# Performance work log

Measured on AMD Instinct MI355X. Metric: run time of the kernel, lower is better.

## Reference

```python
import jax, jax.numpy as jnp
import numpy as np

B, N, DIN, DOUT, H = 4, 2048, 512, 512, 8
HD = DOUT // H


def setup_inputs() -> dict:
    key = jax.random.key(0)
    ks = jax.random.split(key, 8)
    x = jax.random.normal(ks[0], (B, N, DIN), dtype=jnp.float32)
    mask = jax.random.randint(ks[1], (B, 1, N, N), 0, 2, dtype=jnp.int32)
    s = 1.0 / np.sqrt(DIN)
    Wq = jax.random.uniform(ks[2], (DOUT, DIN), jnp.float32, -s, s)
    Wk = jax.random.uniform(ks[3], (DOUT, DIN), jnp.float32, -s, s)
    Wv = jax.random.uniform(ks[4], (DOUT, DIN), jnp.float32, -s, s)
    bq = jax.random.uniform(ks[5], (DOUT,), jnp.float32, -s, s)
    bk = jax.random.uniform(ks[6], (DOUT,), jnp.float32, -s, s)
    bv = jax.random.uniform(ks[7], (DOUT,), jnp.float32, -s, s)
    return {"x": x, "Wq": Wq, "bq": bq, "Wk": Wk, "bk": bk, "Wv": Wv, "bv": bv, "mask": mask}


def reference(x, Wq, bq, Wk, bk, Wv, bv, mask):
    b, n, _ = x.shape
    # torch Linear: y = x @ W.T + b ; split heads -> [b, h, n, hd]
    def proj(W, bias):
        y = jnp.einsum('bnd,od->bno', x, W) + bias
        return y.reshape(b, n, H, HD).transpose(0, 2, 1, 3)
    Q, K, V = proj(Wq, bq), proj(Wk, bk), proj(Wv, bv)
    scores = jnp.einsum('bhnd,bhmd->bhnm', Q, K) / np.sqrt(HD).astype(np.float32)
    scores = jnp.where(mask == 0, jnp.float32(-1e9), scores)
    attn = jax.nn.softmax(scores, axis=-1)
    ctx = jnp.einsum('bhnm,bhmd->bhnd', attn, V)
    ctx = ctx.transpose(0, 2, 1, 3).reshape(b, n, DOUT)
    return jax.nn.elu(ctx)
```

## Files before the change

kernel.cpp:

```cpp
#include <hip/hip_runtime.h>
#include <math.h>
#include <stdint.h>

#define CB 4
#define CN 2048
#define CDIN 512
#define CDOUT 512
#define CH 8
#define CHD 64
#define CM (CB * CN)
#define CBH (CB * CH)
#define NKT (CN / 64)

typedef _Float16 f16x8 __attribute__((ext_vector_type(8)));
typedef _Float16 f16x4 __attribute__((ext_vector_type(4)));
typedef float    f32x4 __attribute__((ext_vector_type(4)));

#define QSCALE 0.1803368801111204f

#define PB_X  2048
#define PB_WQ 2176
#define PB_WK 2304
#define PB_WV 2432
#define PB_MB 3456

__global__ __launch_bounds__(256) void prep_kernel(
    const float* __restrict__ x,  _Float16* __restrict__ xh,
    const float* __restrict__ Wq, _Float16* __restrict__ wqh,
    const float* __restrict__ Wk, _Float16* __restrict__ wkh,
    const float* __restrict__ Wv, _Float16* __restrict__ wvh,
    const int* __restrict__ mask, unsigned long long* __restrict__ mbits)
{
    const int bx = blockIdx.x;
    if (bx >= PB_WV) {
        const int lane = threadIdx.x & 63;
        const int wv   = threadIdx.x >> 6;
        const int wbase = (bx - PB_WV) * 256 + wv * 64;
        unsigned long long myword = 0;
        #pragma unroll 8
        for (int it = 0; it < 64; ++it) {
            int v = mask[(size_t)(wbase + it) * 64 + lane];
            unsigned long long bal = __ballot(v != 0);
            if (lane == it) myword = bal;
        }
        mbits[wbase + lane] = myword;
        return;
    }
    const float* s; _Float16* d; int i;
    if (bx < PB_X)       { s = x;  d = xh;  i = bx * 2048 + threadIdx.x * 8; }
    else if (bx < PB_WQ) { s = Wq; d = wqh; i = (bx - PB_X)  * 2048 + threadIdx.x * 8; }
    else if (bx < PB_WK) { s = Wk; d = wkh; i = (bx - PB_WQ) * 2048 + threadIdx.x * 8; }
    else                 { s = Wv; d = wvh; i = (bx - PB_WK) * 2048 + threadIdx.x * 8; }
    float4 a = *(const float4*)&s[i];
    float4 b = *(const float4*)&s[i + 4];
    f16x8 h = {(_Float16)a.x, (_Float16)a.y, (_Float16)a.z, (_Float16)a.w,
               (_Float16)b.x, (_Float16)b.y, (_Float16)b.z, (_Float16)b.w};
    *(f16x8*)&d[i] = h;
}

__global__ __launch_bounds__(256) void proj_kernel(
    const _Float16* __restrict__ xh,
    const _Float16* __restrict__ Wqh, const float* __restrict__ bq,
    const _Float16* __restrict__ Wkh, const float* __restrict__ bk,
    const _Float16* __restrict__ Wvh, const float* __restrict__ bv,
    _Float16* __restrict__ Qf, _Float16* __restrict__ Kf, _Float16* __restrict__ Vt)
{
    const int z = blockIdx.z;
    const _Float16* W; const float* bias;
    if (z == 0)      { W = Wqh; bias = bq; }
    else if (z == 1) { W = Wkh; bias = bk; }
    else             { W = Wvh; bias = bv; }

    __shared__ _Float16 SM[2 * 128 * 72];

    const int tid  = threadIdx.x;
    const int m0   = blockIdx.x * 128;
    const int o0   = blockIdx.y * 128;
    const int lane = tid & 63, w = tid >> 6;
    const int il   = lane & 15, quad = lane >> 4;
    const int srow = tid >> 3, kc = (tid & 7) * 8;

    f32x4 acc[2][8] = {};
    f16x8 xr[4], wr[4];

    #pragma unroll
    for (int i = 0; i < 4; ++i) {
        xr[i] = *(const f16x8*)&xh[(size_t)(m0 + srow + i * 32) * CDIN + kc];
        wr[i] = *(const f16x8*)&W[(size_t)(o0 + srow + i * 32) * CDIN + kc];
    }

    for (int k0 = 0; k0 < CDIN; k0 += 64) {
        #pragma unroll
        for (int i = 0; i < 4; ++i) {
            *(f16x8*)&SM[(srow + i * 32) * 72 + kc] = xr[i];
            *(f16x8*)&SM[9216 + (srow + i * 32) * 72 + kc] = wr[i];
        }
        __syncthreads();

        if (k0 + 64 < CDIN) {
            #pragma unroll
            for (int i = 0; i < 4; ++i) {
                xr[i] = *(const f16x8*)&xh[(size_t)(m0 + srow + i * 32) * CDIN + k0 + 64 + kc];
                wr[i] = *(const f16x8*)&W[(size_t)(o0 + srow + i * 32) * CDIN + k0 + 64 + kc];
            }
        }

        #pragma unroll
        for (int dh = 0; dh < 2; ++dh) {
            f16x8 X0 = *(const f16x8*)&SM[(w * 32 + il) * 72 + dh * 32 + quad * 8];
            f16x8 X1 = *(const f16x8*)&SM[(w * 32 + 16 + il) * 72 + dh * 32 + quad * 8];
            if (z < 2) {
                #pragma unroll
                for (int s = 0; s < 8; ++s) {
                    f16x8 Wv_ = *(const f16x8*)&SM[9216 + (s * 16 + il) * 72 + dh * 32 + quad * 8];
                    acc[0][s] = __builtin_amdgcn_mfma_f32_16x16x32_f16(Wv_, X0, acc[0][s], 0, 0, 0);
                    acc[1][s] = __builtin_amdgcn_mfma_f32_16x16x32_f16(Wv_, X1, acc[1][s], 0, 0, 0);
                }
            } else {
                #pragma unroll
                for (int s = 0; s < 8; ++s) {
                    f16x8 Wv_ = *(const f16x8*)&SM[9216 + (s * 16 + il) * 72 + dh * 32 + quad * 8];
                    acc[0][s] = __builtin_amdgcn_mfma_f32_16x16x32_f16(X0, Wv_, acc[0][s], 0, 0, 0);
                    acc[1][s] = __builtin_amdgcn_mfma_f32_16x16x32_f16(X1, Wv_, acc[1][s], 0, 0, 0);
                }
            }
        }
        __syncthreads();
    }

    const int b  = m0 / CN;
    const int nb = m0 & (CN - 1);
    if (z < 2) {
        const float sc = (z == 0) ? QSCALE : 1.0f;
        #pragma unroll
        for (int s = 0; s < 8; ++s) {
            #pragma unroll
            for (int mi = 0; mi < 2; ++mi) {
                f16x4 pv;
                #pragma unroll
                for (int r = 0; r < 4; ++r)
                    pv[r] = (_Float16)((acc[mi][s][r] + bias[o0 + s * 16 + quad * 4 + r]) * sc);
                *(f16x4*)&SM[(w * 32 + mi * 16 + il) * 140 + s * 16 + quad * 4] = pv;
            }
        }
    } else {
        #pragma unroll
        for (int s = 0; s < 8; ++s) {
            const float bval = bias[o0 + s * 16 + il];
            #pragma unroll
            for (int mi = 0; mi < 2; ++mi) {
                f16x4 pv = {(_Float16)(acc[mi][s][0] + bval),
                            (_Float16)(acc[mi][s][1] + bval),
                            (_Float16)(acc[mi][s][2] + bval),
                            (_Float16)(acc[mi][s][3] + bval)};
                *(f16x4*)&SM[(s * 16 + il) * 140 + w * 32 + mi * 16 + quad * 4] = pv;
            }
        }
    }
    __syncthreads();

    const int uu   = tid & 127;
    const int hseg = tid >> 7;
    const int bh   = b * CH + (o0 >> 6) + hseg;
    if (z < 2) {
        _Float16* dst = ((z == 0) ? Qf : Kf) + ((size_t)bh * CN + nb) * CHD;
        #pragma unroll
        for (int k = 0; k < 8; ++k) {
            int n = k * 16 + (uu >> 3);
            int d = (uu & 7) * 8;
            *(f16x8*)&dst[(size_t)n * CHD + d] =
                *(const f16x8*)&SM[n * 140 + hseg * 64 + d];
        }
    } else {
        _Float16* dst = Vt + (size_t)bh * CHD * CN + nb;
        #pragma unroll
        for (int k = 0; k < 8; ++k) {
            int d = k * 8 + (uu >> 4);
            int n = (uu & 15) * 8;
            *(f16x8*)&dst[(size_t)d * CN + n] =
                *(const f16x8*)&SM[(hseg * 64 + d) * 140 + n];
        }
    }
}

__global__ __launch_bounds__(512, 4) void attn_kernel(
    const _Float16* __restrict__ Qf, const _Float16* __restrict__ Kf,
    const _Float16* __restrict__ Vt, const unsigned long long* __restrict__ mbits,
    float* __restrict__ out)
{
    __shared__ _Float16 Ks[2][64][72];
    __shared__ _Float16 Vs[2][64][72];
    __shared__ _Float16 Ps[8][16][72];

    const int tid  = threadIdx.x;
    const int q0   = blockIdx.x * 128;
    const int bh   = blockIdx.y;
    const int b    = bh >> 3, h = bh & 7;
    const int lane = tid & 63, w = tid >> 6;
    const int il   = lane & 15, quad = lane >> 4;
    const int srow = tid >> 3, sc0 = (tid & 7) * 8;

    const _Float16* Qb = Qf + (size_t)bh * CN * CHD;
    const _Float16* Kb = Kf + (size_t)bh * CN * CHD;
    const _Float16* Vb = Vt + (size_t)bh * CHD * CN;

    const int qg = q0 + w * 16 + il;
    const unsigned long long* mrow = mbits + ((size_t)b * CN + qg) * NKT;

    f16x8 Qa0 = *(const f16x8*)&Qb[(size_t)qg * CHD + quad * 8];
    f16x8 Qa1 = *(const f16x8*)&Qb[(size_t)qg * CHD + 32 + quad * 8];

    const f16x8 ones = {1.f16, 1.f16, 1.f16, 1.f16, 1.f16, 1.f16, 1.f16, 1.f16};

    f32x4 oacc[4] = {};
    f32x4 lacc = {};

    uint4 kA, vA; unsigned long long mn;
    kA = *(const uint4*)&Kb[(size_t)srow * CHD + sc0];
    vA = *(const uint4*)&Vb[(size_t)srow * CN + sc0];
    mn = mrow[0];
    *(uint4*)&Ks[0][srow][sc0] = kA;
    *(uint4*)&Vs[0][srow][sc0] = vA;
    __syncthreads();

    for (int kt = 0; kt < NKT; ++kt) {
        const int cur = kt & 1;
        const unsigned long long mcur = mn;

        if (kt < NKT - 1) {
            kA = *(const uint4*)&Kb[(size_t)((kt + 1) * 64 + srow) * CHD + sc0];
            vA = *(const uint4*)&Vb[(size_t)srow * CN + (kt + 1) * 64 + sc0];
            mn = mrow[kt + 1];
        }

        f32x4 st[4] = {};
        #pragma unroll
        for (int s = 0; s < 4; ++s) {
            f16x8 A0 = *(const f16x8*)&Ks[cur][s * 16 + il][quad * 8];
            f16x8 A1 = *(const f16x8*)&Ks[cur][s * 16 + il][32 + quad * 8];
            st[s] = __builtin_amdgcn_mfma_f32_16x16x32_f16(A0, Qa0, st[s], 0, 0, 0);
            st[s] = __builtin_amdgcn_mfma_f32_16x16x32_f16(A1, Qa1, st[s], 0, 0, 0);
        }

        const uint32_t mlo = (uint32_t)mcur, mhi = (uint32_t)(mcur >> 32);
        #pragma unroll
        for (int s = 0; s < 4; ++s) {
            const uint32_t mm = (s < 2) ? mlo : mhi;
            const int base = (s & 1) * 16 + quad * 4;
            f16x4 pv;
            #pragma unroll
            for (int r = 0; r < 4; ++r) {
                float sv = ((mm >> (base + r)) & 1u) ? st[s][r] : -1e9f;
                pv[r] = (_Float16)__builtin_amdgcn_exp2f(sv);
            }
            *(f16x4*)&Ps[w][il][s * 16 + quad * 4] = pv;
        }

        f16x8 Pa0 = *(const f16x8*)&Ps[w][il][quad * 8];
        f16x8 Pa1 = *(const f16x8*)&Ps[w][il][32 + quad * 8];
        #pragma unroll
        for (int s = 0; s < 4; ++s) {
            f16x8 B0 = *(const f16x8*)&Vs[cur][s * 16 + il][quad * 8];
            f16x8 B1 = *(const f16x8*)&Vs[cur][s * 16 + il][32 + quad * 8];
            oacc[s] = __builtin_amdgcn_mfma_f32_16x16x32_f16(Pa0, B0, oacc[s], 0, 0, 0);
            oacc[s] = __builtin_amdgcn_mfma_f32_16x16x32_f16(Pa1, B1, oacc[s], 0, 0, 0);
        }
        lacc = __builtin_amdgcn_mfma_f32_16x16x32_f16(Pa0, ones, lacc, 0, 0, 0);
        lacc = __builtin_amdgcn_mfma_f32_16x16x32_f16(Pa1, ones, lacc, 0, 0, 0);

        if (kt < NKT - 1) {
            *(uint4*)&Ks[cur ^ 1][srow][sc0] = kA;
            *(uint4*)&Vs[cur ^ 1][srow][sc0] = vA;
            __syncthreads();
        }
    }

    #pragma unroll
    for (int s = 0; s < 4; ++s) {
        const int d = h * CHD + s * 16 + il;
        #pragma unroll
        for (int r = 0; r < 4; ++r) {
            int n = q0 + w * 16 + quad * 4 + r;
            float c = oacc[s][r] / lacc[r];
            out[((size_t)b * CN + n) * CDOUT + d] = c > 0.f ? c : expm1f(c);
        }
    }
}

extern "C" void kernel_launch(void* const* d_in, const int* in_sizes, int n_in,
                              void* d_out, int out_size, void* d_ws, size_t ws_size,
                              hipStream_t stream) {
    const float* x    = (const float*)d_in[0];
    const float* Wq   = (const float*)d_in[1];
    const float* bq   = (const float*)d_in[2];
    const float* Wk   = (const float*)d_in[3];
    const float* bk   = (const float*)d_in[4];
    const float* Wv   = (const float*)d_in[5];
    const float* bv   = (const float*)d_in[6];
    const int*   mask = (const int*)d_in[7];
    float* out = (float*)d_out;

    const size_t nx = (size_t)CM * CDIN;
    const size_t nw = (size_t)CDOUT * CDIN;
    const size_t nt = (size_t)CBH * CN * CHD;
    _Float16* xh  = (_Float16*)d_ws;
    _Float16* wqh = xh + nx;
    _Float16* wkh = wqh + nw;
    _Float16* wvh = wkh + nw;
    _Float16* Qf  = wvh + nw;
    _Float16* Kf  = Qf + nt;
    _Float16* Vt  = Kf + nt;
    unsigned long long* mbits = (unsigned long long*)(Vt + nt);

    prep_kernel<<<dim3(PB_MB), 256, 0, stream>>>(
        x, xh, Wq, wqh, Wk, wkh, Wv, wvh, mask, mbits);
    proj_kernel<<<dim3(CM / 128, CDOUT / 128, 3), 256, 0, stream>>>(
        xh, wqh, bq, wkh, bk, wvh, bv, Qf, Kf, Vt);
    attn_kernel<<<dim3(CN / 128, CBH), 512, 0, stream>>>(
        Qf, Kf, Vt, mbits, out);
}
```

Measured before the change: 211.0 us.

## Give each attention wave two query tiles and XOR-swizzle shared K/V/P

The attention block drops from 8 to 4 waves. Each wave now handles 32 query rows, two 16-row groups, so every K and V fragment read from shared memory feeds twice as many MFMAs. The padded shared arrays are replaced with unpadded uint4 arrays that use an XOR swizzle, meant to avoid bank conflicts and save LDS space. In exchange each wave holds more accumulator registers, and there are fewer waves per block to hide latency.

```diff
diff --git a/kernel.cpp b/kernel.cpp
--- a/kernel.cpp
+++ b/kernel.cpp
@@ -183,14 +183,14 @@
     }
 }
 
-__global__ __launch_bounds__(512, 4) void attn_kernel(
+__global__ __launch_bounds__(256) void attn_kernel(
     const _Float16* __restrict__ Qf, const _Float16* __restrict__ Kf,
     const _Float16* __restrict__ Vt, const unsigned long long* __restrict__ mbits,
     float* __restrict__ out)
 {
-    __shared__ _Float16 Ks[2][64][72];
-    __shared__ _Float16 Vs[2][64][72];
-    __shared__ _Float16 Ps[8][16][72];
+    __shared__ uint4 Ks4[2][64][8];
+    __shared__ uint4 Vs4[2][64][8];
+    __shared__ uint4 Ps4[4][32][8];
 
     const int tid  = threadIdx.x;
     const int q0   = blockIdx.x * 128;
@@ -198,91 +198,131 @@
     const int b    = bh >> 3, h = bh & 7;
     const int lane = tid & 63, w = tid >> 6;
     const int il   = lane & 15, quad = lane >> 4;
-    const int srow = tid >> 3, sc0 = (tid & 7) * 8;
+    const int i7   = il & 7;
+
+    const int srow = tid >> 2;
+    const int sg   = (tid & 3) * 2;
+    const int sw0  = sg       ^ (srow & 7);
+    const int sw1  = (sg + 1) ^ (srow & 7);
+
+    _Float16* Pw = (_Float16*)&Ps4[w][0][0];
 
     const _Float16* Qb = Qf + (size_t)bh * CN * CHD;
     const _Float16* Kb = Kf + (size_t)bh * CN * CHD;
     const _Float16* Vb = Vt + (size_t)bh * CHD * CN;
 
-    const int qg = q0 + w * 16 + il;
-    const unsigned long long* mrow = mbits + ((size_t)b * CN + qg) * NKT;
-
-    f16x8 Qa0 = *(const f16x8*)&Qb[(size_t)qg * CHD + quad * 8];
-    f16x8 Qa1 = *(const f16x8*)&Qb[(size_t)qg * CHD + 32 + quad * 8];
+    const int qg0 = q0 + w * 32 + il;
+    const int qg1 = qg0 + 16;
+    const unsigned long long* mrow0 = mbits + ((size_t)b * CN + qg0) * NKT;
+    const unsigned long long* mrow1 = mbits + ((size_t)b * CN + qg1) * NKT;
+
+    f16x8 Qa[2][2];
+    Qa[0][0] = *(const f16x8*)&Qb[(size_t)qg0 * CHD + quad * 8];
+    Qa[0][1] = *(const f16x8*)&Qb[(size_t)qg0 * CHD + 32 + quad * 8];
+    Qa[1][0] = *(const f16x8*)&Qb[(size_t)qg1 * CHD + quad * 8];
+    Qa[1][1] = *(const f16x8*)&Qb[(size_t)qg1 * CHD + 32 + quad * 8];
 
     const f16x8 ones = {1.f16, 1.f16, 1.f16, 1.f16, 1.f16, 1.f16, 1.f16, 1.f16};
 
-    f32x4 oacc[4] = {};
-    f32x4 lacc = {};
-
-    uint4 kA, vA; unsigned long long mn;
-    kA = *(const uint4*)&Kb[(size_t)srow * CHD + sc0];
-    vA = *(const uint4*)&Vb[(size_t)srow * CN + sc0];
-    mn = mrow[0];
-    *(uint4*)&Ks[0][srow][sc0] = kA;
-    *(uint4*)&Vs[0][srow][sc0] = vA;
+    f32x4 oacc[2][4] = {};
+    f32x4 lacc[2] = {};
+
+    uint4 kA0, kA1, vA0, vA1;
+    unsigned long long mn0, mn1;
+    kA0 = *(const uint4*)&Kb[(size_t)srow * CHD + sg * 8];
+    kA1 = *(const uint4*)&Kb[(size_t)srow * CHD + sg * 8 + 8];
+    vA0 = *(const uint4*)&Vb[(size_t)srow * CN + sg * 8];
+    vA1 = *(const uint4*)&Vb[(size_t)srow * CN + sg * 8 + 8];
+    mn0 = mrow0[0];
+    mn1 = mrow1[0];
+    Ks4[0][srow][sw0] = kA0; Ks4[0][srow][sw1] = kA1;
+    Vs4[0][srow][sw0] = vA0; Vs4[0][srow][sw1] = vA1;
     __syncthreads();
 
     for (int kt = 0; kt < NKT; ++kt) {
         const int cur = kt & 1;
-        const unsigned long long mcur = mn;
+        const unsigned long long mc0 = mn0, mc1 = mn1;
 
         if (kt < NKT - 1) {
-            kA = *(const uint4*)&Kb[(size_t)((kt + 1) * 64 + srow) * CHD + sc0];
-            vA = *(const uint4*)&Vb[(size_t)srow * CN + (kt + 1) * 64 + sc0];
-            mn = mrow[kt + 1];
-        }
-
-        f32x4 st[4] = {};
+            const size_t ko = (size_t)((kt + 1) * 64 + srow) * CHD + sg * 8;
+            kA0 = *(const uint4*)&Kb[ko];
+            kA1 = *(const uint4*)&Kb[ko + 8];
+            const size_t vo = (size_t)srow * CN + (kt + 1) * 64 + sg * 8;
+            vA0 = *(const uint4*)&Vb[vo];
+            vA1 = *(const uint4*)&Vb[vo + 8];
+            mn0 = mrow0[kt + 1];
+            mn1 = mrow1[kt + 1];
+        }
+
+        f32x4 st[2][4] = {};
         #pragma unroll
         for (int s = 0; s < 4; ++s) {
-            f16x8 A0 = *(const f16x8*)&Ks[cur][s * 16 + il][quad * 8];
-            f16x8 A1 = *(const f16x8*)&Ks[cur][s * 16 + il][32 + quad * 8];
-            st[s] = __builtin_amdgcn_mfma_f32_16x16x32_f16(A0, Qa0, st[s], 0, 0, 0);
-            st[s] = __builtin_amdgcn_mfma_f32_16x16x32_f16(A1, Qa1, st[s], 0, 0, 0);
-        }
-
-        const uint32_t mlo = (uint32_t)mcur, mhi = (uint32_t)(mcur >> 32);
+            f16x8 A0 = *(const f16x8*)&Ks4[cur][s * 16 + il][quad ^ i7];
+            f16x8 A1 = *(const f16x8*)&Ks4[cur][s * 16 + il][(4 + quad) ^ i7];
+            st[0][s] = __builtin_amdgcn_mfma_f32_16x16x32_f16(A0, Qa[0][0], st[0][s], 0, 0, 0);
+            st[0][s] = __builtin_amdgcn_mfma_f32_16x16x32_f16(A1, Qa[0][1], st[0][s], 0, 0, 0);
+            st[1][s] = __builtin_amdgcn_mfma_f32_16x16x32_f16(A0, Qa[1][0], st[1][s], 0, 0, 0);
+            st[1][s] = __builtin_amdgcn_mfma_f32_16x16x32_f16(A1, Qa[1][1], st[1][s], 0, 0, 0);
+        }
+
+        #pragma unroll
+        for (int g = 0; g < 2; ++g) {
+            const unsigned long long mw = g ? mc1 : mc0;
+            const uint32_t mlo = (uint32_t)mw, mhi = (uint32_t)(mw >> 32);
+            #pragma unroll
+            for (int s = 0; s < 4; ++s) {
+                const uint32_t mm = (s < 2) ? mlo : mhi;
+                const int base = ((s & 1) << 4) + quad * 4;
+                f16x4 pv;
+                #pragma unroll
+                for (int r = 0; r < 4; ++r) {
+                    float sv = ((mm >> (base + r)) & 1u) ? st[g][s][r] : -1e9f;
+                    pv[r] = (_Float16)__builtin_amdgcn_exp2f(sv);
+                }
+                const int pg = (s * 2 + (quad >> 1)) ^ i7;
+                *(f16x4*)&Pw[(g * 16 + il) * 64 + pg * 8 + (quad & 1) * 4] = pv;
+            }
+        }
+
+        f16x8 Pa[2][2];
+        #pragma unroll
+        for (int g = 0; g < 2; ++g) {
+            Pa[g][0] = *(const f16x8*)&Pw[(g * 16 + il) * 64 + (quad ^ i7) * 8];
+            Pa[g][1] = *(const f16x8*)&Pw[(g * 16 + il) * 64 + ((4 + quad) ^ i7) * 8];
+        }
         #pragma unroll
         for (int s = 0; s < 4; ++s) {
-            const uint32_t mm = (s < 2) ? mlo : mhi;
-            const int base = (s & 1) * 16 + quad * 4;
-            f16x4 pv;
+            f16x8 B0 = *(const f16x8*)&Vs4[cur][s * 16 + il][quad ^ i7];
+            f16x8 B1 = *(const f16x8*)&Vs4[cur][s * 16 + il][(4 + quad) ^ i7];
+            oacc[0][s] = __builtin_amdgcn_mfma_f32_16x16x32_f16(Pa[0][0], B0, oacc[0][s], 0, 0, 0);
+            oacc[0][s] = __builtin_amdgcn_mfma_f32_16x16x32_f16(Pa[0][1], B1, oacc[0][s], 0, 0, 0);
+            oacc[1][s] = __builtin_amdgcn_mfma_f32_16x16x32_f16(Pa[1][0], B0, oacc[1][s], 0, 0, 0);
+            oacc[1][s] = __builtin_amdgcn_mfma_f32_16x16x32_f16(Pa[1][1], B1, oacc[1][s], 0, 0, 0);
+        }
+        lacc[0] = __builtin_amdgcn_mfma_f32_16x16x32_f16(Pa[0][0], ones, lacc[0], 0, 0, 0);
+        lacc[0] = __builtin_amdgcn_mfma_f32_16x16x32_f16(Pa[0][1], ones, lacc[0], 0, 0, 0);
+        lacc[1] = __builtin_amdgcn_mfma_f32_16x16x32_f16(Pa[1][0], ones, lacc[1], 0, 0, 0);
+        lacc[1] = __builtin_amdgcn_mfma_f32_16x16x32_f16(Pa[1][1], ones, lacc[1], 0, 0, 0);
+
+        if (kt < NKT - 1) {
+            const int nxt = cur ^ 1;
+            Ks4[nxt][srow][sw0] = kA0; Ks4[nxt][srow][sw1] = kA1;
+            Vs4[nxt][srow][sw0] = vA0; Vs4[nxt][srow][sw1] = vA1;
+            __syncthreads();
+        }
+    }
+
+    #pragma unroll
+    for (int g = 0; g < 2; ++g) {
+        #pragma unroll
+        for (int s = 0; s < 4; ++s) {
+            const int d = h * CHD + s * 16 + il;
             #pragma unroll
             for (int r = 0; r < 4; ++r) {
-                float sv = ((mm >> (base + r)) & 1u) ? st[s][r] : -1e9f;
-                pv[r] = (_Float16)__builtin_amdgcn_exp2f(sv);
-            }
-            *(f16x4*)&Ps[w][il][s * 16 + quad * 4] = pv;
-        }
-
-        f16x8 Pa0 = *(const f16x8*)&Ps[w][il][quad * 8];
-        f16x8 Pa1 = *(const f16x8*)&Ps[w][il][32 + quad * 8];
-        #pragma unroll
-        for (int s = 0; s < 4; ++s) {
-            f16x8 B0 = *(const f16x8*)&Vs[cur][s * 16 + il][quad * 8];
-            f16x8 B1 = *(const f16x8*)&Vs[cur][s * 16 + il][32 + quad * 8];
-            oacc[s] = __builtin_amdgcn_mfma_f32_16x16x32_f16(Pa0, B0, oacc[s], 0, 0, 0);
-            oacc[s] = __builtin_amdgcn_mfma_f32_16x16x32_f16(Pa1, B1, oacc[s], 0, 0, 0);
-        }
-        lacc = __builtin_amdgcn_mfma_f32_16x16x32_f16(Pa0, ones, lacc, 0, 0, 0);
-        lacc = __builtin_amdgcn_mfma_f32_16x16x32_f16(Pa1, ones, lacc, 0, 0, 0);
-
-        if (kt < NKT - 1) {
-            *(uint4*)&Ks[cur ^ 1][srow][sc0] = kA;
-            *(uint4*)&Vs[cur ^ 1][srow][sc0] = vA;
-            __syncthreads();
-        }
-    }
-
-    #pragma unroll
-    for (int s = 0; s < 4; ++s) {
-        const int d = h * CHD + s * 16 + il;
-        #pragma unroll
-        for (int r = 0; r < 4; ++r) {
-            int n = q0 + w * 16 + quad * 4 + r;
-            float c = oacc[s][r] / lacc[r];
-            out[((size_t)b * CN + n) * CDOUT + d] = c > 0.f ? c : expm1f(c);
+                int n = q0 + w * 32 + g * 16 + quad * 4 + r;
+                float c = oacc[g][s][r] / lacc[g][r];
+                out[((size_t)b * CN + n) * CDOUT + d] = c > 0.f ? c : expm1f(c);
+            }
         }
     }
 }
@@ -316,6 +356,6 @@
         x, xh, Wq, wqh, Wk, wkh, Wv, wvh, mask, mbits);
     proj_kernel<<<dim3(CM / 128, CDOUT / 128, 3), 256, 0, stream>>>(
         xh, wqh, bq, wkh, bk, wvh, bv, Qf, Kf, Vt);
-    attn_kernel<<<dim3(CN / 128, CBH), 512, 0, stream>>>(
+    attn_kernel<<<dim3(CN / 128, CBH), 256, 0, stream>>>(
         Qf, Kf, Vt, mbits, out);
 }
```

After: 217.7 us. +3.2%, slower.
